# Optimization experiments

Measured on AMD Instinct MI355X. Metric: run time of the kernel, lower is better.

The kernel has to match this reference:

```python
import jax, jax.numpy as jnp
import numpy as np

ROPE_BASE = 100.0


def _rope1d(tok, pos):
    # tok: [B, H, N, d], pos: [B, N] int. Matches croco apply_rope1d.
    d = tok.shape[-1]
    inv_freq = 1.0 / (ROPE_BASE ** (jnp.arange(0, d, 2, dtype=jnp.float32) / d))  # [d/2]
    ang = pos[:, None, :, None].astype(jnp.float32) * inv_freq  # [B,1,N,d/2]
    ang = jnp.concatenate([ang, ang], axis=-1)  # [B,1,N,d]
    cos, sin = jnp.cos(ang).astype(tok.dtype), jnp.sin(ang).astype(tok.dtype)
    x1, x2 = tok[..., : d // 2], tok[..., d // 2 :]
    rot = jnp.concatenate([-x2, x1], axis=-1)  # rotate_half
    return tok * cos + rot * sin


def _rope2d(tok, pos):
    # tok: [B, H, N, D]; first half of D uses pos[...,0] (y), second half pos[...,1] (x)
    y, x = jnp.split(tok, 2, axis=-1)
    return jnp.concatenate([_rope1d(y, pos[..., 0]), _rope1d(x, pos[..., 1])], axis=-1)


def setup_inputs() -> dict:
    key = jax.random.key(0)
    ks = jax.random.split(key, 10)
    B, N, C = 8, 1024, 768
    s = 0.02
    return {
        "query": jax.random.normal(ks[0], (B, N, C), jnp.float32),
        "key": jax.random.normal(ks[1], (B, N, C), jnp.float32),
        "value": jax.random.normal(ks[2], (B, N, C), jnp.float32),
        "qpos": jax.random.randint(ks[3], (B, N, 2), 0, 32, jnp.int32),
        "kpos": jax.random.randint(ks[4], (B, N, 2), 0, 32, jnp.int32),
        "Wq": jax.random.normal(ks[5], (C, C), jnp.float32) * s,
        "Wk": jax.random.normal(ks[6], (C, C), jnp.float32) * s,
        "Wv": jax.random.normal(ks[7], (C, C), jnp.float32) * s,
        "Wo": jax.random.normal(ks[8], (C, C), jnp.float32) * s,
        "bo": jnp.zeros((C,), jnp.float32),
    }


def reference(query, key, value, qpos, kpos, Wq, Wk, Wv, Wo, bo):
    B, Nq, C = query.shape
    H = 12
    hd = C // H
    scale = hd ** -0.5
    # projections (torch Linear: x @ W^T), then split heads -> [B,H,N,hd]
    q = jnp.einsum("bnc,dc->bnd", query, Wq).reshape(B, Nq, H, hd).transpose(0, 2, 1, 3)
    k = jnp.einsum("bnc,dc->bnd", key, Wk).reshape(B, -1, H, hd).transpose(0, 2, 1, 3)
    v = jnp.einsum("bnc,dc->bnd", value, Wv).reshape(B, -1, H, hd).transpose(0, 2, 1, 3)
    q = _rope2d(q, qpos)
    k = _rope2d(k, kpos)
    attn = jnp.einsum("bhqd,bhkd->bhqk", q, k) * scale
    attn = jax.nn.softmax(attn, axis=-1)
    x = jnp.einsum("bhqk,bhkd->bhqd", attn, v)
    x = x.transpose(0, 2, 1, 3).reshape(B, Nq, C)
    return jnp.einsum("bnc,dc->bnd", x, Wo) + bo
```

## Files before the change

### kernel.cpp

```cpp
#include <hip/hip_runtime.h>
#include <hip/hip_bf16.h>
#include <hip/hip_fp16.h>

#define B_DIM 8
#define N_DIM 1024
#define C_DIM 768
#define H_DIM 12
#define HD    64
#define M_DIM (B_DIM * N_DIM)
#define BH    (B_DIM * H_DIM)

static constexpr size_t TEN = (size_t)M_DIM * C_DIM;
static constexpr size_t WN  = (size_t)C_DIM * C_DIM;

typedef __attribute__((ext_vector_type(8))) short    s16x8;
typedef __attribute__((ext_vector_type(8))) _Float16 f16x8;
typedef __attribute__((ext_vector_type(4))) float    f32x4;

__device__ __forceinline__ unsigned short f2h(float f) {
    __half h = __float2half(f);
    return __half_as_ushort(h);
}


__global__ __launch_bounds__(256)
void convX(const float* __restrict__ q, const float* __restrict__ k,
           const float* __restrict__ v, unsigned short* __restrict__ XS)
{
    const int t  = blockIdx.z;
    const int p  = blockIdx.y;
    const int kb = blockIdx.x;
    const float* src = (t == 0) ? q : (t == 1 ? k : v);
    unsigned short* dst = XS + (size_t)t * TEN;

    const int mr = threadIdx.x & 127;
    const int gh = threadIdx.x >> 7;
    const float* s = src + ((size_t)(p * 128 + mr)) * C_DIM + kb * 32 + gh * 16;
    float4 v0 = *(const float4*)(s);
    float4 v1 = *(const float4*)(s + 4);
    float4 v2 = *(const float4*)(s + 8);
    float4 v3 = *(const float4*)(s + 12);
    float f[16] = {v0.x,v0.y,v0.z,v0.w, v1.x,v1.y,v1.z,v1.w,
                   v2.x,v2.y,v2.z,v2.w, v3.x,v3.y,v3.z,v3.w};
    #pragma unroll
    for (int gj = 0; gj < 2; ++gj) {
        int gg = gh * 2 + gj;
        s16x8 h8;
        #pragma unroll
        for (int e = 0; e < 8; ++e)
            h8[e] = (short)f2h(f[gj * 8 + e]);
        size_t a = ((((size_t)p * 24 + kb) * 4 + gg) * 128 + mr) * 8;
        *(s16x8*)(dst + a) = h8;
    }
}

__global__ __launch_bounds__(256)
void convW(const float* __restrict__ wq, const float* __restrict__ wk,
           const float* __restrict__ wv, const float* __restrict__ wo,
           unsigned short* __restrict__ WS, float2* __restrict__ tab)
{
    if (blockIdx.x == 0 && blockIdx.y == 0 && blockIdx.z == 0) {
        #pragma unroll
        for (int i = 0; i < 2; ++i) {
            int t = threadIdx.x + i * 256;
            int pos = t >> 4, j = t & 15;
            float ang = (float)pos * exp2f(-(float)j * 0.41524101186092029f);
            float s, c;
            sincosf(ang, &s, &c);
            tab[t] = make_float2(c, s);
        }
    }

    const int t  = blockIdx.z;
    const int p  = blockIdx.y;
    const int kb = blockIdx.x;
    const float* src = (t == 0) ? wq : (t == 1 ? wk : (t == 2 ? wv : wo));
    unsigned short* dst = WS + (size_t)t * WN;

    const int mr = threadIdx.x & 127;
    const int gh = threadIdx.x >> 7;
    const float* s = src + ((size_t)(p * 128 + mr)) * C_DIM + kb * 32 + gh * 16;
    float4 v0 = *(const float4*)(s);
    float4 v1 = *(const float4*)(s + 4);
    float4 v2 = *(const float4*)(s + 8);
    float4 v3 = *(const float4*)(s + 12);
    float f[16] = {v0.x,v0.y,v0.z,v0.w, v1.x,v1.y,v1.z,v1.w,
                   v2.x,v2.y,v2.z,v2.w, v3.x,v3.y,v3.z,v3.w};
    #pragma unroll
    for (int gj = 0; gj < 2; ++gj) {
        int gg = gh * 2 + gj;
        s16x8 h8;
        #pragma unroll
        for (int e = 0; e < 8; ++e)
            h8[e] = (short)f2h(f[gj * 8 + e]);
        size_t a = ((((size_t)p * 24 + kb) * 4 + gg) * 128 + mr) * 8;
        *(s16x8*)(dst + a) = h8;
    }
}

template<int MODE>
__global__ __launch_bounds__(256)
void gemmF(const unsigned short* __restrict__ XQ, const unsigned short* __restrict__ XK,
           const unsigned short* __restrict__ XV,
           const unsigned short* __restrict__ WQ, const unsigned short* __restrict__ WK,
           const unsigned short* __restrict__ WV,
           const int* __restrict__ qpos, const int* __restrict__ kpos,
           const float2* __restrict__ tab,
           unsigned short* __restrict__ OQ, unsigned short* __restrict__ OK_,
           unsigned short* __restrict__ OV,
           const float* __restrict__ bias, float* __restrict__ Of)
{
    extern __shared__ unsigned short smem_us[];
    auto sA = reinterpret_cast<unsigned short (*)[4][128][8]>(smem_us);
    auto sB = reinterpret_cast<unsigned short (*)[4][128][8]>(smem_us + 8192);

    const int tid  = threadIdx.x;
    const int lane = tid & 63;
    const int w    = tid >> 6;
    const int wr   = w >> 1, wc = w & 1;
    const int c    = lane & 15, g = lane >> 4;

    const int chunk = gridDim.x >> 3;
    const int wgid  = (blockIdx.x & 7) * chunk + (blockIdx.x >> 3);
    int z, m0, n0;
    if (MODE == 1) {
        z = wgid / 384;
        int r = wgid - z * 384;
        m0 = (r / 6) * 128;
        n0 = (r % 6) * 128;
    } else {
        z = 0;
        m0 = (wgid / 6) * 128;
        n0 = (wgid % 6) * 128;
    }

    const unsigned short *Ap, *Bp;
    if (MODE == 0 || z == 0) { Ap = XQ; Bp = WQ; }
    else if (z == 1)         { Ap = XK; Bp = WK; }
    else                     { Ap = XV; Bp = WV; }

    const size_t abase0 = (size_t)(m0 >> 7) * 24 * 4096;
    const size_t bbase0 = (size_t)(n0 >> 7) * 24 * 4096;

    f32x4 acc[4][4] = {};

    auto stage = [&](int kb, int buf) {
        #pragma unroll
        for (int t = 0; t < 4; ++t) {
            int is = w * 4 + t;
            int sel = is >> 3;
            int j   = is & 7;
            int gg  = j >> 1, half = j & 1;
            const unsigned short* srcp =
                (sel ? Bp + bbase0 : Ap + abase0) + (size_t)kb * 4096
                + (size_t)gg * 1024 + (half * 64 + lane) * 8;
            unsigned short* dstp = sel ? &sB[buf][gg][half * 64][0]
                                       : &sA[buf][gg][half * 64][0];
            __builtin_amdgcn_global_load_lds(
                (const __attribute__((address_space(1))) void*)srcp,
                (__attribute__((address_space(3))) void*)dstp,
                16, 0, 0);
        }
    };

    stage(0, 0);
    stage(1, 1);

    for (int kb = 0; kb < 24; ++kb) {
        int buf = kb & 1;
        if (kb < 23) asm volatile("s_waitcnt vmcnt(4)" ::: "memory");
        else         asm volatile("s_waitcnt vmcnt(0)" ::: "memory");
        __builtin_amdgcn_sched_barrier(0);
        __builtin_amdgcn_s_barrier();
        __builtin_amdgcn_sched_barrier(0);

        f16x8 a[4], b[4];
        #pragma unroll
        for (int mi = 0; mi < 4; ++mi)
            a[mi] = *(const f16x8*)&sA[buf][g][wr * 64 + 16 * mi + c][0];
        #pragma unroll
        for (int ni = 0; ni < 4; ++ni)
            b[ni] = *(const f16x8*)&sB[buf][g][wc * 64 + 16 * ni + c][0];
        __builtin_amdgcn_s_setprio(1);
        #pragma unroll
        for (int mi = 0; mi < 4; ++mi)
            #pragma unroll
            for (int ni = 0; ni < 4; ++ni)
                acc[mi][ni] = __builtin_amdgcn_mfma_f32_16x16x32_f16(a[mi], b[ni], acc[mi][ni], 0, 0, 0);
        __builtin_amdgcn_s_setprio(0);

        __builtin_amdgcn_sched_barrier(0);
        __builtin_amdgcn_s_barrier();
        __builtin_amdgcn_sched_barrier(0);
        if (kb + 2 < 24) stage(kb + 2, buf);
    }

    if (MODE == 0) {
        #pragma unroll
        for (int ni = 0; ni < 4; ++ni) {
            int d = n0 + wc * 64 + 16 * ni + c;
            float bv = bias[d];
            #pragma unroll
            for (int mi = 0; mi < 4; ++mi)
                #pragma unroll
                for (int r = 0; r < 4; ++r) {
                    int m = m0 + wr * 64 + 16 * mi + 4 * g + r;
                    Of[(size_t)m * C_DIM + d] = acc[mi][ni][r] + bv;
                }
        }
    } else if (z == 2) {
        __syncthreads();
        auto T = reinterpret_cast<unsigned short (*)[132]>(smem_us);
        #pragma unroll
        for (int ni = 0; ni < 4; ++ni) {
            int dl = wc * 64 + 16 * ni + c;
            #pragma unroll
            for (int mi = 0; mi < 4; ++mi) {
                int ml = wr * 64 + 16 * mi + 4 * g;
                unsigned short hs[4];
                #pragma unroll
                for (int r = 0; r < 4; ++r)
                    hs[r] = f2h(acc[mi][ni][r]);
                *(uint2*)&T[dl][ml] =
                    make_uint2((unsigned)hs[0] | ((unsigned)hs[1] << 16),
                               (unsigned)hs[2] | ((unsigned)hs[3] << 16));
            }
        }
        __syncthreads();
        const int b = m0 >> 10, nbase = m0 & 1023;
        #pragma unroll
        for (int it = 0; it < 8; ++it) {
            int f  = tid + it * 256;
            int dl = f >> 4;
            int mc = (f & 15) * 8;
            s16x8 vv = *(const s16x8*)&T[dl][mc];
            int d = n0 + dl, h = d >> 6, dh = d & 63;
            *(s16x8*)(OV + ((size_t)(b * H_DIM + h) * HD + dh) * N_DIM + nbase + mc) = vv;
        }
    } else {
        const int* P = z ? kpos : qpos;
        unsigned short* T = z ? OK_ : OQ;
        const float scale = z ? 1.0f : 0.18033688011112042f;
        const int hh = (n0 >> 6) + wc;
        #pragma unroll
        for (int mi = 0; mi < 4; ++mi)
            #pragma unroll
            for (int r = 0; r < 4; ++r) {
                int m = m0 + wr * 64 + 16 * mi + 4 * g + r;
                int b = m >> 10, n = m & 1023;
                size_t base = ((size_t)(b * H_DIM + hh) * N_DIM + n) * HD;
                #pragma unroll
                for (int bb = 0; bb < 2; ++bb) {
                    int pos = P[2 * m + bb];
                    float2 cs = tab[pos * 16 + c];
                    float x1 = acc[mi][bb * 2 + 0][r];
                    float x2 = acc[mi][bb * 2 + 1][r];
                    float r1 = (x1 * cs.x - x2 * cs.y) * scale;
                    float r2 = (x2 * cs.x + x1 * cs.y) * scale;
                    T[base + bb * 32 + c]      = f2h(r1);
                    T[base + bb * 32 + 16 + c] = f2h(r2);
                }
            }
    }
}

__global__ __launch_bounds__(256)
void attn_f16(const unsigned short* __restrict__ Qh, const unsigned short* __restrict__ Kh,
              const unsigned short* __restrict__ Vt,
              unsigned short* __restrict__ Xb)
{
    __shared__ _Float16 sK[64][72];
    __shared__ _Float16 sV[64][72];
    __shared__ _Float16 sP[4][2][16][72];

    const int tid  = threadIdx.x;
    const int lane = tid & 63;
    const int wv   = tid >> 6;
    const int c    = lane & 15;
    const int g    = lane >> 4;

    const int bid   = blockIdx.x;
    const int xcd   = bid & 7;
    const int local = bid >> 3;
    const int bh    = xcd * 12 + (local >> 3);
    const int q0    = (local & 7) * 128;
    const size_t hb = (size_t)bh * (N_DIM * HD);

    const size_t qoffA = hb + (size_t)(q0 + wv * 32 + c) * HD;
    const size_t qoffB = qoffA + (size_t)16 * HD;
    f16x8 qA0 = *(const f16x8*)(Qh + qoffA + 8 * g);
    f16x8 qA1 = *(const f16x8*)(Qh + qoffA + 32 + 8 * g);
    f16x8 qB0 = *(const f16x8*)(Qh + qoffB + 8 * g);
    f16x8 qB1 = *(const f16x8*)(Qh + qoffB + 32 + 8 * g);

    f16x8 ones;
    #pragma unroll
    for (int e = 0; e < 8; ++e) ones[e] = (_Float16)1.0f;

    f32x4 accA[4] = {}, accB[4] = {};
    f32x4 lAcc[2] = {};

    const int f0 = tid, f1 = tid + 256;
    const int row0 = f0 >> 3, ch0 = (f0 & 7) * 8;
    const int row1 = f1 >> 3, ch1 = (f1 & 7) * 8;
    const unsigned short* Kbase = Kh + hb;
    const unsigned short* Vbase = Vt + hb;

    s16x8 rK0 = *(const s16x8*)(Kbase + (size_t)row0 * HD + ch0);
    s16x8 rK1 = *(const s16x8*)(Kbase + (size_t)row1 * HD + ch1);
    s16x8 rV0 = *(const s16x8*)(Vbase + (size_t)row0 * N_DIM + ch0);
    s16x8 rV1 = *(const s16x8*)(Vbase + (size_t)row1 * N_DIM + ch1);

    for (int kt = 0; kt < 16; ++kt) {
        __builtin_amdgcn_s_barrier();

        *(s16x8*)&sK[row0][ch0] = rK0;
        *(s16x8*)&sK[row1][ch1] = rK1;
        *(s16x8*)&sV[row0][ch0] = rV0;
        *(s16x8*)&sV[row1][ch1] = rV1;

        if (kt < 15) {
            rK0 = *(const s16x8*)(Kbase + (size_t)((kt + 1) * 64 + row0) * HD + ch0);
            rK1 = *(const s16x8*)(Kbase + (size_t)((kt + 1) * 64 + row1) * HD + ch1);
            rV0 = *(const s16x8*)(Vbase + (size_t)row0 * N_DIM + (kt + 1) * 64 + ch0);
            rV1 = *(const s16x8*)(Vbase + (size_t)row1 * N_DIM + (kt + 1) * 64 + ch1);
        }

        asm volatile("s_waitcnt lgkmcnt(0)" ::: "memory");
        __builtin_amdgcn_sched_barrier(0);
        __builtin_amdgcn_s_barrier();
        __builtin_amdgcn_sched_barrier(0);

        f32x4 sA[4] = {}, sB[4] = {};
        __builtin_amdgcn_s_setprio(1);
        #pragma unroll
        for (int st = 0; st < 4; ++st) {
            f16x8 a0 = *(const f16x8*)&sK[16 * st + c][8 * g];
            f16x8 a1 = *(const f16x8*)&sK[16 * st + c][32 + 8 * g];
            sA[st] = __builtin_amdgcn_mfma_f32_16x16x32_f16(a0, qA0, sA[st], 0, 0, 0);
            sA[st] = __builtin_amdgcn_mfma_f32_16x16x32_f16(a1, qA1, sA[st], 0, 0, 0);
            sB[st] = __builtin_amdgcn_mfma_f32_16x16x32_f16(a0, qB0, sB[st], 0, 0, 0);
            sB[st] = __builtin_amdgcn_mfma_f32_16x16x32_f16(a1, qB1, sB[st], 0, 0, 0);
        }
        __builtin_amdgcn_s_setprio(0);

        #pragma unroll
        for (int st = 0; st < 4; ++st) {
            float pA[4], pB[4];
            #pragma unroll
            for (int r = 0; r < 4; ++r) {
                pA[r] = __builtin_amdgcn_exp2f(sA[st][r]);
                pB[r] = __builtin_amdgcn_exp2f(sB[st][r]);
            }
            __half2 a01 = __float22half2_rn(make_float2(pA[0], pA[1]));
            __half2 a23 = __float22half2_rn(make_float2(pA[2], pA[3]));
            __half2 b01 = __float22half2_rn(make_float2(pB[0], pB[1]));
            __half2 b23 = __float22half2_rn(make_float2(pB[2], pB[3]));
            *(uint2*)&sP[wv][0][c][16 * st + 4 * g] =
                make_uint2(*(unsigned*)&a01, *(unsigned*)&a23);
            *(uint2*)&sP[wv][1][c][16 * st + 4 * g] =
                make_uint2(*(unsigned*)&b01, *(unsigned*)&b23);
        }

        __builtin_amdgcn_s_setprio(1);
        #pragma unroll
        for (int m = 0; m < 2; ++m) {
            f16x8 pbA = *(const f16x8*)&sP[wv][0][c][32 * m + 8 * g];
            f16x8 pbB = *(const f16x8*)&sP[wv][1][c][32 * m + 8 * g];
            #pragma unroll
            for (int sd = 0; sd < 4; ++sd) {
                f16x8 va = *(const f16x8*)&sV[16 * sd + c][32 * m + 8 * g];
                accA[sd] = __builtin_amdgcn_mfma_f32_16x16x32_f16(va, pbA, accA[sd], 0, 0, 0);
                accB[sd] = __builtin_amdgcn_mfma_f32_16x16x32_f16(va, pbB, accB[sd], 0, 0, 0);
            }
            lAcc[0] = __builtin_amdgcn_mfma_f32_16x16x32_f16(ones, pbA, lAcc[0], 0, 0, 0);
            lAcc[1] = __builtin_amdgcn_mfma_f32_16x16x32_f16(ones, pbB, lAcc[1], 0, 0, 0);
        }
        __builtin_amdgcn_s_setprio(0);
    }

    float invA = 1.0f / lAcc[0][0];
    float invB = 1.0f / lAcc[1][0];

    const int b = bh / H_DIM, h = bh % H_DIM;
    #pragma unroll
    for (int sub = 0; sub < 2; ++sub) {
        const f32x4* acc = sub ? accB : accA;
        float invl = sub ? invB : invA;
        const int q = q0 + wv * 32 + sub * 16 + c;
        const int m  = b * N_DIM + q;
        const int p_ = m >> 7, mr = m & 127;
        #pragma unroll
        for (int sd = 0; sd < 4; ++sd) {
            int kdim = h * 64 + 16 * sd + 4 * g;
            int kb = kdim >> 5;
            int gg = (kdim >> 3) & 3;
            int e  = kdim & 7;
            size_t a = ((((size_t)p_ * 24 + kb) * 4 + gg) * 128 + mr) * 8 + e;
            unsigned short hs[4];
            #pragma unroll
            for (int r = 0; r < 4; ++r)
                hs[r] = f2h(acc[sd][r] * invl);
            *(uint2*)(Xb + a) =
                make_uint2((unsigned)hs[0] | ((unsigned)hs[1] << 16),
                           (unsigned)hs[2] | ((unsigned)hs[3] << 16));
        }
    }
}

extern "C" void kernel_launch(void* const* d_in, const int* in_sizes, int n_in,
                              void* d_out, int out_size, void* d_ws, size_t ws_size,
                              hipStream_t stream)
{
    const float* query = (const float*)d_in[0];
    const float* key_  = (const float*)d_in[1];
    const float* value = (const float*)d_in[2];
    const int*   qpos  = (const int*)d_in[3];
    const int*   kpos  = (const int*)d_in[4];
    const float* Wq    = (const float*)d_in[5];
    const float* Wk    = (const float*)d_in[6];
    const float* Wv    = (const float*)d_in[7];
    const float* Wo    = (const float*)d_in[8];
    const float* bo    = (const float*)d_in[9];
    float* out = (float*)d_out;

    unsigned short* XS  = (unsigned short*)d_ws;
    unsigned short* WS  = XS + 3 * TEN;
    unsigned short* Qh  = WS + 4 * WN;
    unsigned short* Kh  = Qh + TEN;
    unsigned short* Vt  = Kh + TEN;
    unsigned short* Xb  = Vt + TEN;
    float2* tab = (float2*)(Xb + TEN);

    convX<<<dim3(24, 64, 3), 256, 0, stream>>>(query, key_, value, XS);
    convW<<<dim3(24, 6, 4), 256, 0, stream>>>(Wq, Wk, Wv, Wo, WS, tab);

    gemmF<1><<<dim3(1152), 256, 33792, stream>>>(
        XS + 0 * TEN, XS + 1 * TEN, XS + 2 * TEN,
        WS + 0 * WN, WS + 1 * WN, WS + 2 * WN,
        qpos, kpos, tab, Qh, Kh, Vt, nullptr, nullptr);

    attn_f16<<<dim3(768), 256, 0, stream>>>(Qh, Kh, Vt, Xb);

    gemmF<0><<<dim3(384), 256, 32768, stream>>>(
        Xb, nullptr, nullptr,
        WS + 3 * WN, nullptr, nullptr,
        nullptr, nullptr, nullptr, nullptr, nullptr, nullptr, bo, out);
}
```

Measured before the change: 131.4 us.

## Fuse fp32-to-fp16 activation conversion into QKV projection GEMM loads

```diff
diff --git a/kernel.cpp b/kernel.cpp
--- a/kernel.cpp
+++ b/kernel.cpp
@@ -22,16 +22,39 @@
     return __half_as_ushort(h);
 }
 
+__device__ __forceinline__ f16x8 cvt8(float4 a, float4 b) {
+    __half2 h0 = __float22half2_rn(make_float2(a.x, a.y));
+    __half2 h1 = __float22half2_rn(make_float2(a.z, a.w));
+    __half2 h2 = __float22half2_rn(make_float2(b.x, b.y));
+    __half2 h3 = __float22half2_rn(make_float2(b.z, b.w));
+    union { f16x8 v; __half2 h[4]; } u;
+    u.h[0] = h0; u.h[1] = h1; u.h[2] = h2; u.h[3] = h3;
+    return u.v;
+}
+
 
 __global__ __launch_bounds__(256)
-void convX(const float* __restrict__ q, const float* __restrict__ k,
-           const float* __restrict__ v, unsigned short* __restrict__ XS)
+void convW(const float* __restrict__ wq, const float* __restrict__ wk,
+           const float* __restrict__ wv, const float* __restrict__ wo,
+           unsigned short* __restrict__ WS, float2* __restrict__ tab)
 {
+    if (blockIdx.x == 0 && blockIdx.y == 0 && blockIdx.z == 0) {
+        #pragma unroll
+        for (int i = 0; i < 2; ++i) {
+            int t = threadIdx.x + i * 256;
+            int pos = t >> 4, j = t & 15;
+            float ang = (float)pos * exp2f(-(float)j * 0.41524101186092029f);
+            float s, c;
+            sincosf(ang, &s, &c);
+            tab[t] = make_float2(c, s);
+        }
+    }
+
     const int t  = blockIdx.z;
     const int p  = blockIdx.y;
     const int kb = blockIdx.x;
-    const float* src = (t == 0) ? q : (t == 1 ? k : v);
-    unsigned short* dst = XS + (size_t)t * TEN;
+    const float* src = (t == 0) ? wq : (t == 1 ? wk : (t == 2 ? wv : wo));
+    unsigned short* dst = WS + (size_t)t * WN;
 
     const int mr = threadIdx.x & 127;
     const int gh = threadIdx.x >> 7;
@@ -54,54 +77,11 @@
     }
 }
 
-__global__ __launch_bounds__(256)
-void convW(const float* __restrict__ wq, const float* __restrict__ wk,
-           const float* __restrict__ wv, const float* __restrict__ wo,
-           unsigned short* __restrict__ WS, float2* __restrict__ tab)
-{
-    if (blockIdx.x == 0 && blockIdx.y == 0 && blockIdx.z == 0) {
-        #pragma unroll
-        for (int i = 0; i < 2; ++i) {
-            int t = threadIdx.x + i * 256;
-            int pos = t >> 4, j = t & 15;
-            float ang = (float)pos * exp2f(-(float)j * 0.41524101186092029f);
-            float s, c;
-            sincosf(ang, &s, &c);
-            tab[t] = make_float2(c, s);
-        }
-    }
-
-    const int t  = blockIdx.z;
-    const int p  = blockIdx.y;
-    const int kb = blockIdx.x;
-    const float* src = (t == 0) ? wq : (t == 1 ? wk : (t == 2 ? wv : wo));
-    unsigned short* dst = WS + (size_t)t * WN;
-
-    const int mr = threadIdx.x & 127;
-    const int gh = threadIdx.x >> 7;
-    const float* s = src + ((size_t)(p * 128 + mr)) * C_DIM + kb * 32 + gh * 16;
-    float4 v0 = *(const float4*)(s);
-    float4 v1 = *(const float4*)(s + 4);
-    float4 v2 = *(const float4*)(s + 8);
-    float4 v3 = *(const float4*)(s + 12);
-    float f[16] = {v0.x,v0.y,v0.z,v0.w, v1.x,v1.y,v1.z,v1.w,
-                   v2.x,v2.y,v2.z,v2.w, v3.x,v3.y,v3.z,v3.w};
-    #pragma unroll
-    for (int gj = 0; gj < 2; ++gj) {
-        int gg = gh * 2 + gj;
-        s16x8 h8;
-        #pragma unroll
-        for (int e = 0; e < 8; ++e)
-            h8[e] = (short)f2h(f[gj * 8 + e]);
-        size_t a = ((((size_t)p * 24 + kb) * 4 + gg) * 128 + mr) * 8;
-        *(s16x8*)(dst + a) = h8;
-    }
-}
-
 template<int MODE>
 __global__ __launch_bounds__(256)
-void gemmF(const unsigned short* __restrict__ XQ, const unsigned short* __restrict__ XK,
-           const unsigned short* __restrict__ XV,
+void gemmF(const float* __restrict__ AfQ, const float* __restrict__ AfK,
+           const float* __restrict__ AfV,
+           const unsigned short* __restrict__ XA,
            const unsigned short* __restrict__ WQ, const unsigned short* __restrict__ WK,
            const unsigned short* __restrict__ WV,
            const int* __restrict__ qpos, const int* __restrict__ kpos,
@@ -134,65 +114,137 @@
         n0 = (wgid % 6) * 128;
     }
 
-    const unsigned short *Ap, *Bp;
-    if (MODE == 0 || z == 0) { Ap = XQ; Bp = WQ; }
-    else if (z == 1)         { Ap = XK; Bp = WK; }
-    else                     { Ap = XV; Bp = WV; }
-
-    const size_t abase0 = (size_t)(m0 >> 7) * 24 * 4096;
+    const unsigned short* Bp = (MODE == 0 || z == 0) ? WQ : (z == 1 ? WK : WV);
     const size_t bbase0 = (size_t)(n0 >> 7) * 24 * 4096;
 
     f32x4 acc[4][4] = {};
 
-    auto stage = [&](int kb, int buf) {
-        #pragma unroll
-        for (int t = 0; t < 4; ++t) {
-            int is = w * 4 + t;
-            int sel = is >> 3;
-            int j   = is & 7;
-            int gg  = j >> 1, half = j & 1;
-            const unsigned short* srcp =
-                (sel ? Bp + bbase0 : Ap + abase0) + (size_t)kb * 4096
+    auto stageB = [&](int kb, int buf) {
+        #pragma unroll
+        for (int t = 0; t < 2; ++t) {
+            int j = w * 2 + t;
+            int gg = j >> 1, half = j & 1;
+            const unsigned short* srcp = Bp + bbase0 + (size_t)kb * 4096
                 + (size_t)gg * 1024 + (half * 64 + lane) * 8;
-            unsigned short* dstp = sel ? &sB[buf][gg][half * 64][0]
-                                       : &sA[buf][gg][half * 64][0];
             __builtin_amdgcn_global_load_lds(
                 (const __attribute__((address_space(1))) void*)srcp,
-                (__attribute__((address_space(3))) void*)dstp,
+                (__attribute__((address_space(3))) void*)&sB[buf][gg][half * 64][0],
                 16, 0, 0);
         }
     };
 
-    stage(0, 0);
-    stage(1, 1);
-
-    for (int kb = 0; kb < 24; ++kb) {
-        int buf = kb & 1;
-        if (kb < 23) asm volatile("s_waitcnt vmcnt(4)" ::: "memory");
-        else         asm volatile("s_waitcnt vmcnt(0)" ::: "memory");
+    if constexpr (MODE == 1) {
+        const float* Af = (z == 0) ? AfQ : (z == 1 ? AfK : AfV);
+        const int arow = tid & 127;
+        const int ah   = tid >> 7;
+        const float* Abase = Af + (size_t)(m0 + arow) * C_DIM + ah * 16;
+
+        f16x8 Ra[2], Rb[2];
+        auto loadA = [&](int kb, f16x8* R) {
+            const float* s = Abase + kb * 32;
+            float4 v0 = *(const float4*)(s);
+            float4 v1 = *(const float4*)(s + 4);
+            float4 v2 = *(const float4*)(s + 8);
+            float4 v3 = *(const float4*)(s + 12);
+            R[0] = cvt8(v0, v1);
+            R[1] = cvt8(v2, v3);
+        };
+        auto writeA = [&](const f16x8* R, int buf) {
+            *(f16x8*)&sA[buf][2 * ah + 0][arow][0] = R[0];
+            *(f16x8*)&sA[buf][2 * ah + 1][arow][0] = R[1];
+        };
+
+        loadA(0, Ra);
+        loadA(1, Rb);
+        stageB(0, 0);
+        stageB(1, 1);
+        writeA(Ra, 0);
+        asm volatile("s_waitcnt vmcnt(2)" ::: "memory");
+        asm volatile("s_waitcnt lgkmcnt(0)" ::: "memory");
         __builtin_amdgcn_sched_barrier(0);
         __builtin_amdgcn_s_barrier();
         __builtin_amdgcn_sched_barrier(0);
 
-        f16x8 a[4], b[4];
-        #pragma unroll
-        for (int mi = 0; mi < 4; ++mi)
-            a[mi] = *(const f16x8*)&sA[buf][g][wr * 64 + 16 * mi + c][0];
-        #pragma unroll
-        for (int ni = 0; ni < 4; ++ni)
-            b[ni] = *(const f16x8*)&sB[buf][g][wc * 64 + 16 * ni + c][0];
-        __builtin_amdgcn_s_setprio(1);
-        #pragma unroll
-        for (int mi = 0; mi < 4; ++mi)
+        auto iter = [&](int kb, f16x8* Rwr , f16x8* Rld ) {
+            int buf = kb & 1;
+            if (kb + 1 < 24) writeA(Rwr, buf ^ 1);
+            if (kb + 2 < 24) loadA(kb + 2, Rld);
+
+            f16x8 a[4], b[4];
+            #pragma unroll
+            for (int mi = 0; mi < 4; ++mi)
+                a[mi] = *(const f16x8*)&sA[buf][g][wr * 64 + 16 * mi + c][0];
             #pragma unroll
             for (int ni = 0; ni < 4; ++ni)
-                acc[mi][ni] = __builtin_amdgcn_mfma_f32_16x16x32_f16(a[mi], b[ni], acc[mi][ni], 0, 0, 0);
-        __builtin_amdgcn_s_setprio(0);
-
-        __builtin_amdgcn_sched_barrier(0);
-        __builtin_amdgcn_s_barrier();
-        __builtin_amdgcn_sched_barrier(0);
-        if (kb + 2 < 24) stage(kb + 2, buf);
+                b[ni] = *(const f16x8*)&sB[buf][g][wc * 64 + 16 * ni + c][0];
+            __builtin_amdgcn_s_setprio(1);
+            #pragma unroll
+            for (int mi = 0; mi < 4; ++mi)
+                #pragma unroll
+                for (int ni = 0; ni < 4; ++ni)
+                    acc[mi][ni] = __builtin_amdgcn_mfma_f32_16x16x32_f16(a[mi], b[ni], acc[mi][ni], 0, 0, 0);
+            __builtin_amdgcn_s_setprio(0);
+
+            if (kb + 1 < 24) {
+                if (kb + 2 < 24) asm volatile("s_waitcnt vmcnt(4)" ::: "memory");
+                else             asm volatile("s_waitcnt vmcnt(0)" ::: "memory");
+                asm volatile("s_waitcnt lgkmcnt(0)" ::: "memory");
+                __builtin_amdgcn_sched_barrier(0);
+                __builtin_amdgcn_s_barrier();
+                __builtin_amdgcn_sched_barrier(0);
+                if (kb + 2 < 24) stageB(kb + 2, buf);
+            }
+        };
+        #pragma unroll 1
+        for (int kb2 = 0; kb2 < 24; kb2 += 2) {
+            iter(kb2 + 0, Rb, Ra);
+            iter(kb2 + 1, Ra, Rb);
+        }
+    } else {
+        const size_t abase0 = (size_t)(m0 >> 7) * 24 * 4096;
+        auto stageA = [&](int kb, int buf) {
+            #pragma unroll
+            for (int t = 0; t < 2; ++t) {
+                int j = w * 2 + t;
+                int gg = j >> 1, half = j & 1;
+                const unsigned short* srcp = XA + abase0 + (size_t)kb * 4096
+                    + (size_t)gg * 1024 + (half * 64 + lane) * 8;
+                __builtin_amdgcn_global_load_lds(
+                    (const __attribute__((address_space(1))) void*)srcp,
+                    (__attribute__((address_space(3))) void*)&sA[buf][gg][half * 64][0],
+                    16, 0, 0);
+            }
+        };
+        stageA(0, 0); stageB(0, 0);
+        stageA(1, 1); stageB(1, 1);
+        for (int kb = 0; kb < 24; ++kb) {
+            int buf = kb & 1;
+            if (kb < 23) asm volatile("s_waitcnt vmcnt(4)" ::: "memory");
+            else         asm volatile("s_waitcnt vmcnt(0)" ::: "memory");
+            __builtin_amdgcn_sched_barrier(0);
+            __builtin_amdgcn_s_barrier();
+            __builtin_amdgcn_sched_barrier(0);
+
+            f16x8 a[4], b[4];
+            #pragma unroll
+            for (int mi = 0; mi < 4; ++mi)
+                a[mi] = *(const f16x8*)&sA[buf][g][wr * 64 + 16 * mi + c][0];
+            #pragma unroll
+            for (int ni = 0; ni < 4; ++ni)
+                b[ni] = *(const f16x8*)&sB[buf][g][wc * 64 + 16 * ni + c][0];
+            __builtin_amdgcn_s_setprio(1);
+            #pragma unroll
+            for (int mi = 0; mi < 4; ++mi)
+                #pragma unroll
+                for (int ni = 0; ni < 4; ++ni)
+                    acc[mi][ni] = __builtin_amdgcn_mfma_f32_16x16x32_f16(a[mi], b[ni], acc[mi][ni], 0, 0, 0);
+            __builtin_amdgcn_s_setprio(0);
+
+            __builtin_amdgcn_sched_barrier(0);
+            __builtin_amdgcn_s_barrier();
+            __builtin_amdgcn_sched_barrier(0);
+            if (kb + 2 < 24) { stageA(kb + 2, buf); stageB(kb + 2, buf); }
+        }
     }
 
     if (MODE == 0) {
@@ -424,26 +476,24 @@
     const float* bo    = (const float*)d_in[9];
     float* out = (float*)d_out;
 
-    unsigned short* XS  = (unsigned short*)d_ws;
-    unsigned short* WS  = XS + 3 * TEN;
+    unsigned short* WS  = (unsigned short*)d_ws;
     unsigned short* Qh  = WS + 4 * WN;
     unsigned short* Kh  = Qh + TEN;
     unsigned short* Vt  = Kh + TEN;
     unsigned short* Xb  = Vt + TEN;
     float2* tab = (float2*)(Xb + TEN);
 
-    convX<<<dim3(24, 64, 3), 256, 0, stream>>>(query, key_, value, XS);
     convW<<<dim3(24, 6, 4), 256, 0, stream>>>(Wq, Wk, Wv, Wo, WS, tab);
 
     gemmF<1><<<dim3(1152), 256, 33792, stream>>>(
-        XS + 0 * TEN, XS + 1 * TEN, XS + 2 * TEN,
+        query, key_, value, nullptr,
         WS + 0 * WN, WS + 1 * WN, WS + 2 * WN,
         qpos, kpos, tab, Qh, Kh, Vt, nullptr, nullptr);
 
     attn_f16<<<dim3(768), 256, 0, stream>>>(Qh, Kh, Vt, Xb);
 
     gemmF<0><<<dim3(384), 256, 32768, stream>>>(
-        Xb, nullptr, nullptr,
+        nullptr, nullptr, nullptr, Xb,
         WS + 3 * WN, nullptr, nullptr,
         nullptr, nullptr, nullptr, nullptr, nullptr, nullptr, bo, out);
 }
```

Result: slower. 155.4 us (+18.3%).
